# Performance work log

Measured on AMD Instinct MI355X. Metric: run time of the kernel, lower is better.

The kernel has to match this reference:

```python
import jax, jax.numpy as jnp
import numpy as np

DT = 0.1
T_END = 1.0
# matches python `int(t[-1] // dt)` in etd_integration
N_STEPS = int(T_END // DT)


def _expm(X, order=10, squarings=4):
    """Scaling-and-squaring Taylor matrix exponential (fixed order, jit-safe,
    differentiable). Accurate here because ||X|| is kept small by construction."""
    n = X.shape[0]
    I = jnp.eye(n, dtype=X.dtype)
    Xs = X / (2.0 ** squarings)
    term, acc = I, I
    for k in range(1, order + 1):
        term = (term @ Xs) / k
        acc = acc + term
    for _ in range(squarings):
        acc = acc @ acc
    return acc


def etd1_bch2(A, B, dt):
    """ETD1 propagators for dX/dt = A X + X B + N:
    m1_L = e^{dt A}, m1_R = e^{dt B}, m2 = A^{-1}(e^{dt A} - I) (phi1 weight)."""
    m1_L = _expm(dt * A)
    m1_R = _expm(dt * B)
    m2 = jnp.linalg.solve(A, m1_L - jnp.eye(A.shape[0], dtype=A.dtype))
    return m1_L, m1_R, m2


def reference(x, x0, adj, alpha_train, w, d):
    n = adj.shape[0]
    alph = jax.nn.sigmoid(alpha_train)[:, None]          # [n,1]
    d_c = jnp.clip(d, 0.0, 1.0)                          # [2h]
    w_mat = (w * d_c) @ w.T                              # [2h,2h]
    A = alph * 0.5 * adj - alph * 0.5 * jnp.eye(n, dtype=adj.dtype)   # [n,n]
    B = w_mat - jnp.eye(w_mat.shape[0], dtype=w_mat.dtype)            # [2h,2h]
    m1_L, m1_R, m2 = etd1_bch2(A, B, DT)
    forcing = m2 @ x0                                     # constant per step

    def step(IC, _):
        return m1_L @ IC @ m1_R + forcing, None

    z, _ = jax.lax.scan(step, x, None, length=N_STEPS)
    return z


def setup_inputs() -> dict:
    key = jax.random.key(0)
    ks = jax.random.split(key, 6)
    n, dfeat = 2048, 1024
    x = jax.random.normal(ks[0], (n, dfeat), dtype=jnp.float32)
    x0 = jax.random.normal(ks[1], (n, dfeat), dtype=jnp.float32)
    # normalized-adjacency stand-in: uniform entries scaled by 1/n (row sums ~0.5)
    adj = jax.random.uniform(ks[2], (n, n), dtype=jnp.float32) / n
    alpha_train = jax.random.normal(ks[3], (n,), dtype=jnp.float32)
    # original inits w = eye(2h); perturb slightly so math is nontrivial but e^{dtB} stays tame
    w = jnp.eye(dfeat, dtype=jnp.float32) + 0.02 * jax.random.normal(ks[4], (dfeat, dfeat), dtype=jnp.float32)
    d = jax.random.uniform(ks[5], (dfeat,), dtype=jnp.float32)
    return {"x": x, "x0": x0, "adj": adj, "alpha_train": alpha_train, "w": w, "d": d}
```

## Files before the change

kernel.cpp:

```cpp
#include <hip/hip_runtime.h>

typedef __attribute__((ext_vector_type(8))) short short8v;
typedef __attribute__((ext_vector_type(4))) float f32x4;

typedef const __attribute__((address_space(1))) void gvoid_t;
typedef __attribute__((address_space(3))) void svoid_t;

__device__ __forceinline__ unsigned short f2b(float f) {
    unsigned u = __float_as_uint(f);
    unsigned r = (u + 0x7fffu + ((u >> 16) & 1u)) >> 16;
    return (unsigned short)r;
}
__device__ __forceinline__ float b2f(unsigned short h) {
    return __uint_as_float((unsigned)h << 16);
}


__global__ void k_build_A(const float* __restrict__ adj,
                          const float* __restrict__ alpha,
                          float* __restrict__ Xs, unsigned short* __restrict__ Xb,
                          int n, float scale)
{
    int j = blockIdx.x * 256 + threadIdx.x;
    int i = blockIdx.y;
    if (j >= n) return;
    size_t idx = (size_t)i * n + j;
    float s = 1.f / (1.f + expf(-alpha[i]));
    float v = scale * s * (adj[idx] - (i == j ? 1.f : 0.f));
    Xs[idx] = v;
    Xb[idx] = f2b(v);
}

__global__ void k_build_EW(const float* __restrict__ w,
                           const float* __restrict__ d,
                           unsigned short* __restrict__ Eb,
                           unsigned short* __restrict__ Edb,
                           float* __restrict__ Edf, int h)
{
    int j = blockIdx.x * 256 + threadIdx.x;
    int i = blockIdx.y;
    if (j >= h) return;
    size_t idx = (size_t)i * h + j;
    float e = w[idx] - (i == j ? 1.f : 0.f);
    float dc = fminf(fmaxf(d[j], 0.f), 1.f);
    Eb[idx] = f2b(e);
    float ed = e * dc;
    Edb[idx] = f2b(ed);
    Edf[idx] = ed;
}

__global__ void k_build_R(const float* __restrict__ Ed,
                          const float* __restrict__ d,
                          float* __restrict__ R, int h, float dt)
{
    __shared__ float tile[32][33];
    int bx = blockIdx.x * 32, by = blockIdx.y * 32;
    int tx = threadIdx.x, ty = threadIdx.y;
    #pragma unroll
    for (int r = 0; r < 32; r += 8)
        tile[ty + r][tx] = Ed[(size_t)(bx + ty + r) * h + by + tx];
    __syncthreads();
    #pragma unroll
    for (int r = 0; r < 32; r += 8) {
        int i = by + ty + r, j = bx + tx;
        float v = Ed[(size_t)i * h + j] + tile[tx][ty + r];
        if (i == j) v += fminf(fmaxf(d[i], 0.f), 1.f) - 1.f;
        R[(size_t)i * h + j] = dt * v;
    }
}

__global__ void k_tsplit(const float* __restrict__ in,
                         unsigned short* __restrict__ outT, int R, int C)
{
    __shared__ float tile[32][33];
    int bx = blockIdx.x * 32, by = blockIdx.y * 32;
    int tx = threadIdx.x, ty = threadIdx.y;
    #pragma unroll
    for (int r = 0; r < 32; r += 8)
        tile[ty + r][tx] = in[(size_t)(by + ty + r) * C + bx + tx];
    __syncthreads();
    #pragma unroll
    for (int r = 0; r < 32; r += 8)
        outT[(size_t)(bx + ty + r) * R + by + tx] = f2b(tile[tx][ty + r]);
}


template<int FM, int FN, int MW>
__global__ __launch_bounds__(256, MW)
void gemm_bf16(const unsigned short* __restrict__ A,
               const unsigned short* __restrict__ BT,
               float* __restrict__ C,
               float* __restrict__ C2,
               unsigned short* __restrict__ Cb,
               unsigned short* __restrict__ Cb2,
               unsigned short* __restrict__ Cb3,
               unsigned short* __restrict__ CbT,
               const float* __restrict__ D,
               const float* __restrict__ D2,
               const unsigned short* __restrict__ Db,
               int M, int N, int K,
               float alpha, float beta, float g2, float g3,
               float pa, float pb, float pc,
               float qa, float qb, float qc)
{
    constexpr int BM = FM * 32, BN = FN * 32, BK = 64;
    constexpr int AIT = BM * BK / (8 * 256);
    constexpr int BIT = BN * BK / (8 * 256);
    constexpr int LPT = AIT + BIT;
    __shared__ unsigned short As[2][BM * BK];
    __shared__ unsigned short Bs[2][BN * BK];

    int bid = blockIdx.y * gridDim.x + blockIdx.x;
    int rpx = gridDim.y >> 3;
    int q = bid & 7, c = bid >> 3;
    int by = q * rpx + (c % rpx);
    int bx = c / rpx;

    const int tid  = threadIdx.x;
    const int lane = tid & 63;
    const int wave = tid >> 6;
    const int wr = wave >> 1, wc = wave & 1;
    const int l16 = lane & 15, l4 = lane >> 4;
    const int brow = by * BM, bcol = bx * BN;

    f32x4 acc[FM][FN];
    #pragma unroll
    for (int m = 0; m < FM; ++m)
        #pragma unroll
        for (int j = 0; j < FN; ++j)
            acc[m][j] = (f32x4){0.f, 0.f, 0.f, 0.f};

    const unsigned short* Ab = A + (size_t)brow * K;
    const unsigned short* Bb = BT + (size_t)bcol * K;
    const int nt = K / BK;

    auto stage = [&](int b, int k0) {
        #pragma unroll
        for (int it = 0; it < AIT; ++it) {
            int cb = it * 256 + wave * 64;
            int ch = cb + lane;
            int r = ch >> 3, cc = ch & 7;
            int cs = cc ^ (r & 7);
            __builtin_amdgcn_global_load_lds(
                (gvoid_t*)(Ab + (size_t)r * K + k0 + cs * 8),
                (svoid_t*)(&As[b][cb * 8]), 16, 0, 0);
        }
        #pragma unroll
        for (int it = 0; it < BIT; ++it) {
            int cb = it * 256 + wave * 64;
            int ch = cb + lane;
            int r = ch >> 3, cc = ch & 7;
            int cs = cc ^ (r & 7);
            __builtin_amdgcn_global_load_lds(
                (gvoid_t*)(Bb + (size_t)r * K + k0 + cs * 8),
                (svoid_t*)(&Bs[b][cb * 8]), 16, 0, 0);
        }
    };

    stage(0, 0);
    stage(1, BK);

    for (int t = 0; t < nt; ++t) {
        const int cur = t & 1;
        if (t + 1 < nt) {
            asm volatile("s_waitcnt vmcnt(%0)" :: "i"(LPT) : "memory");
        } else {
            asm volatile("s_waitcnt vmcnt(0)" ::: "memory");
        }
        __builtin_amdgcn_s_barrier();
        asm volatile("" ::: "memory");
        __builtin_amdgcn_sched_barrier(0);

        short8v af[FM][2], bf[FN][2];
        #pragma unroll
        for (int m = 0; m < FM; ++m) {
            int r = wr * FM * 16 + m * 16 + l16;
            #pragma unroll
            for (int hf = 0; hf < 2; ++hf) {
                int cs = (hf * 4 + l4) ^ (r & 7);
                af[m][hf] = *(const short8v*)&As[cur][r * BK + cs * 8];
            }
        }
        #pragma unroll
        for (int j = 0; j < FN; ++j) {
            int r = wc * FN * 16 + j * 16 + l16;
            #pragma unroll
            for (int hf = 0; hf < 2; ++hf) {
                int cs = (hf * 4 + l4) ^ (r & 7);
                bf[j][hf] = *(const short8v*)&Bs[cur][r * BK + cs * 8];
            }
        }
        __builtin_amdgcn_s_setprio(1);
        #pragma unroll
        for (int hf = 0; hf < 2; ++hf)
            #pragma unroll
            for (int m = 0; m < FM; ++m)
                #pragma unroll
                for (int j = 0; j < FN; ++j)
                    acc[m][j] = __builtin_amdgcn_mfma_f32_16x16x32_bf16(
                        af[m][hf], bf[j][hf], acc[m][j], 0, 0, 0);
        __builtin_amdgcn_s_setprio(0);
        __builtin_amdgcn_sched_barrier(0);
        __builtin_amdgcn_s_barrier();
        asm volatile("" ::: "memory");
        if (t + 2 < nt) stage(cur, (t + 2) * BK);
    }

    #pragma unroll
    for (int m = 0; m < FM; ++m) {
        #pragma unroll
        for (int j = 0; j < FN; ++j) {
            const int row0 = brow + wr * FM * 16 + m * 16 + l4 * 4;
            const int col  = bcol + wc * FN * 16 + j * 16 + l16;
            float vv[4];
            #pragma unroll
            for (int q2 = 0; q2 < 4; ++q2) {
                size_t idx = (size_t)(row0 + q2) * N + col;
                float a0 = acc[m][j][q2];
                float v = alpha * a0;
                float dv = 0.f, dbv = 0.f;
                if (D)  { dv = D[idx]; v = fmaf(beta, dv, v); }
                if (D2) v = fmaf(g2, D2[idx], v);
                if (Db) { dbv = b2f(Db[idx]); v = fmaf(g3, dbv, v); }
                vv[q2] = v;
                if (C)  C[idx] = v;
                if (Cb) Cb[idx] = f2b(v);
                if (C2 || Cb2) {
                    float v2 = pa * a0;
                    if (D)  v2 = fmaf(pb, dv, v2);
                    if (Db) v2 = fmaf(pc, dbv, v2);
                    if (C2)  C2[idx] = v2;
                    if (Cb2) Cb2[idx] = f2b(v2);
                }
                if (Cb3) {
                    float v3 = qa * a0;
                    if (D)  v3 = fmaf(qb, dv, v3);
                    if (Db) v3 = fmaf(qc, dbv, v3);
                    Cb3[idx] = f2b(v3);
                }
            }
            if (CbT) {
                ushort4 t4;
                t4.x = f2b(vv[0]); t4.y = f2b(vv[1]);
                t4.z = f2b(vv[2]); t4.w = f2b(vv[3]);
                *reinterpret_cast<ushort4*>(&CbT[(size_t)col * M + row0]) = t4;
            }
        }
    }
}


extern "C" void kernel_launch(void* const* d_in, const int* in_sizes, int n_in,
                              void* d_out, int out_size, void* d_ws, size_t ws_size,
                              hipStream_t stream)
{
    const float* x     = (const float*)d_in[0];
    const float* x0    = (const float*)d_in[1];
    const float* adj   = (const float*)d_in[2];
    const float* alpha = (const float*)d_in[3];
    const float* w     = (const float*)d_in[4];
    const float* dvec  = (const float*)d_in[5];

    const int n = in_sizes[3];
    const int h = in_sizes[5];
    const size_t MB = 1u << 20;
    char* ws = (char*)d_ws;

    typedef unsigned short u16;
    float* Xs    = (float*)(ws + 0 * MB);
    u16*   XAb   = (u16*)(ws + 16 * MB);
    u16*   XAT   = (u16*)(ws + 24 * MB);
    u16*   Mah   = (u16*)(ws + 32 * MB);
    u16*   Pmb   = (u16*)(ws + 40 * MB);
    u16*   M3ah  = (u16*)(ws + 48 * MB);
    u16*   MbT   = (u16*)(ws + 56 * MB);
    u16*   M3bTb = (u16*)(ws + 58 * MB);
    u16*   Eb_   = (u16*)(ws + 0 * MB);
    u16*   Edb   = (u16*)(ws + 2 * MB);
    float* Edf   = (float*)(ws + 4 * MB);
    float* R     = (float*)(ws + 8 * MB);
    float* XBf   = (float*)(ws + 12 * MB);
    u16*   XBb   = (u16*)(ws + 16 * MB);
    u16*   XBT   = (u16*)(ws + 18 * MB);
    float* P2f   = (float*)(ws + 20 * MB);
    u16*   P2b   = (u16*)(ws + 24 * MB);
    float* P3f   = (float*)(ws + 26 * MB);
    u16*   P3b   = (u16*)(ws + 30 * MB);
    u16*   x0T   = (u16*)(ws + 0 * MB);
    float* Ff    = (float*)(ws + 4 * MB);
    u16*   FTb   = (u16*)(ws + 12 * MB);
    float* uf    = (float*)(ws + 16 * MB);
    u16*   ub    = (u16*)(ws + 24 * MB);
    float* F2f   = (float*)(ws + 60 * MB);
    u16*   F2Tb  = (u16*)(ws + 12 * MB);
    float* vf    = (float*)(ws + 16 * MB);
    u16*   vb    = (u16*)(ws + 24 * MB);
    float* F3f   = (float*)(ws + 40 * MB);
    u16*   zt    = (u16*)(ws + 68 * MB);
    float* tf    = (float*)(ws + 0 * MB);
    u16*   tb16  = (u16*)(ws + 8 * MB);
    float* za    = (float*)(ws + 16 * MB);

    const dim3 blk(256);
    const dim3 gNN(n / 32, n / 64);
    const dim3 gHN(h / 32, n / 64);
    const dim3 gHH(h / 64, h / 32);
    const float dt = 0.1f;
    const u16* nu16 = nullptr;
    const float* nf32 = nullptr;

    k_build_A<<<dim3(n / 256, n), blk, 0, stream>>>(adj, alpha, Xs, XAb, n, 0.5f * dt);
    k_tsplit<<<dim3(n / 32, n / 32), dim3(32, 8), 0, stream>>>(Xs, XAT, n, n);
    gemm_bf16<2, 1, 4><<<gNN, blk, 0, stream>>>(
        XAb, XAT, nullptr, nullptr, Mah, Pmb, M3ah, nullptr, Xs, nf32, nu16,
        n, n, n, 0.5f, 1.f, 0.f, 0.f,
        1.f / 6.f, 0.5f, 0.f, 4.5f, 3.f, 0.f);

    k_build_EW<<<dim3(h / 256, h), blk, 0, stream>>>(w, dvec, Eb_, Edb, Edf, h);
    k_build_R<<<dim3(h / 32, h / 32), dim3(32, 8), 0, stream>>>(Edf, dvec, R, h, dt);
    gemm_bf16<1, 2, 4><<<gHH, blk, 0, stream>>>(
        Edb, Eb_, XBf, nullptr, XBb, nullptr, nullptr, XBT, R, nf32, nu16,
        h, h, h, dt, 1.f, 0.f, 0.f, 0.f, 0.f, 0.f, 0.f, 0.f, 0.f);
    gemm_bf16<1, 2, 4><<<gHH, blk, 0, stream>>>(
        XBb, XBT, P2f, nullptr, P2b, nullptr, nullptr, nullptr, nf32, nf32, nu16,
        h, h, h, 1.f, 0.f, 0.f, 0.f, 0.f, 0.f, 0.f, 0.f, 0.f, 0.f);
    gemm_bf16<1, 2, 4><<<gHH, blk, 0, stream>>>(
        P2b, XBT, nullptr, P3f, nullptr, P3b, nullptr, MbT, XBf, P2f, nu16,
        h, h, h, 1.f / 6.f, 1.f, 0.5f, 0.f, 1.f, 0.f, 0.f, 0.f, 0.f, 0.f);
    gemm_bf16<1, 2, 4><<<gHH, blk, 0, stream>>>(
        P3b, XBT, nullptr, nullptr, nullptr, nullptr, nullptr, M3bTb,
        P3f, P2f, XBb,
        h, h, h, 3.375f, 4.5f, 4.5f, 3.f, 0.f, 0.f, 0.f, 0.f, 0.f, 0.f);

    k_tsplit<<<dim3(h / 32, n / 32), dim3(32, 8), 0, stream>>>(x0, x0T, n, h);
    gemm_bf16<2, 1, 4><<<gHN, blk, 0, stream>>>(
        Pmb, x0T, Ff, nullptr, nullptr, nullptr, nullptr, FTb, x0, nf32, nu16,
        n, h, n, dt, dt, 0.f, 0.f, 0.f, 0.f, 0.f, 0.f, 0.f, 0.f);
    gemm_bf16<2, 1, 4><<<gHN, blk, 0, stream>>>(
        Mah, FTb, uf, nullptr, ub, nullptr, nullptr, nullptr, Ff, nf32, nu16,
        n, h, n, 1.f, 1.f, 0.f, 0.f, 0.f, 0.f, 0.f, 0.f, 0.f, 0.f);
    gemm_bf16<2, 1, 4><<<gHN, blk, 0, stream>>>(
        ub, MbT, F2f, nullptr, nullptr, nullptr, nullptr, F2Tb, uf, Ff, nu16,
        n, h, h, 1.f, 1.f, 1.f, 0.f, 0.f, 0.f, 0.f, 0.f, 0.f, 0.f);
    gemm_bf16<2, 1, 4><<<gHN, blk, 0, stream>>>(
        Mah, F2Tb, vf, nullptr, vb, nullptr, nullptr, nullptr, F2f, nf32, nu16,
        n, h, n, 1.f, 1.f, 0.f, 0.f, 0.f, 0.f, 0.f, 0.f, 0.f, 0.f);
    gemm_bf16<2, 1, 4><<<gHN, blk, 0, stream>>>(
        vb, MbT, F3f, nullptr, nullptr, nullptr, nullptr, nullptr, vf, Ff, nu16,
        n, h, h, 1.f, 1.f, 1.f, 0.f, 0.f, 0.f, 0.f, 0.f, 0.f, 0.f);

    k_tsplit<<<dim3(h / 32, n / 32), dim3(32, 8), 0, stream>>>(x, zt, n, h);
    const float* zf = x;
    for (int s = 0; s < 3; ++s) {
        gemm_bf16<2, 1, 4><<<gHN, blk, 0, stream>>>(
            M3ah, zt, tf, nullptr, tb16, nullptr, nullptr, nullptr, zf, nf32, nu16,
            n, h, n, 1.f, 1.f, 0.f, 0.f, 0.f, 0.f, 0.f, 0.f, 0.f, 0.f);
        float* zout = (s == 2) ? (float*)d_out : za;
        gemm_bf16<2, 1, 4><<<gHN, blk, 0, stream>>>(
            tb16, M3bTb, zout, nullptr, nullptr, nullptr, nullptr,
            (s == 2) ? nullptr : zt, tf, F3f, nu16,
            n, h, h, 1.f, 1.f, 1.f, 0.f, 0.f, 0.f, 0.f, 0.f, 0.f, 0.f);
        zf = za;
    }
}
```

Measured before the change: 353.0 us.

## Fuse A build with transpose, merge x/x0 transposes, read bf16 epilogue operands

Builds the scaled A matrix and its bf16 transpose in a single tiled kernel instead of writing an fp32 copy and transposing it separately. The x0 and x transposes are merged into one launch. Several GEMM epilogues now take the bf16 residual copy instead of fp32 intermediates, so fp32 outputs such as uf, vf and tf are no longer written or read. The n×n GEMM moves to a 2×2 fragment tile, and workspace offsets are repacked. This cuts memory traffic and launch count, but residual terms are now added at bf16 rather than fp32 precision, which costs accuracy.

```diff
diff --git a/kernel.cpp b/kernel.cpp
--- a/kernel.cpp
+++ b/kernel.cpp
@@ -16,19 +16,27 @@
 }
 
 
-__global__ void k_build_A(const float* __restrict__ adj,
-                          const float* __restrict__ alpha,
-                          float* __restrict__ Xs, unsigned short* __restrict__ Xb,
-                          int n, float scale)
-{
-    int j = blockIdx.x * 256 + threadIdx.x;
-    int i = blockIdx.y;
-    if (j >= n) return;
-    size_t idx = (size_t)i * n + j;
-    float s = 1.f / (1.f + expf(-alpha[i]));
-    float v = scale * s * (adj[idx] - (i == j ? 1.f : 0.f));
-    Xs[idx] = v;
-    Xb[idx] = f2b(v);
+__global__ void k_build_AT(const float* __restrict__ adj,
+                           const float* __restrict__ alpha,
+                           unsigned short* __restrict__ XAb,
+                           unsigned short* __restrict__ XATb,
+                           int n, float scale)
+{
+    __shared__ float tile[32][33];
+    int bx = blockIdx.x * 32, by = blockIdx.y * 32;
+    int tx = threadIdx.x, ty = threadIdx.y;
+    #pragma unroll
+    for (int r = 0; r < 32; r += 8) {
+        int i = by + ty + r, j = bx + tx;
+        float s = 1.f / (1.f + expf(-alpha[i]));
+        float v = scale * s * (adj[(size_t)i * n + j] - (i == j ? 1.f : 0.f));
+        XAb[(size_t)i * n + j] = f2b(v);
+        tile[ty + r][tx] = v;
+    }
+    __syncthreads();
+    #pragma unroll
+    for (int r = 0; r < 32; r += 8)
+        XATb[(size_t)(bx + ty + r) * n + by + tx] = f2b(tile[tx][ty + r]);
 }
 
 __global__ void k_build_EW(const float* __restrict__ w,
@@ -69,19 +77,29 @@
     }
 }
 
-__global__ void k_tsplit(const float* __restrict__ in,
-                         unsigned short* __restrict__ outT, int R, int C)
+__global__ void k_tsplit2(const float* __restrict__ in0,
+                          const float* __restrict__ in1,
+                          unsigned short* __restrict__ out0,
+                          unsigned short* __restrict__ out1, int R, int C)
 {
     __shared__ float tile[32][33];
     int bx = blockIdx.x * 32, by = blockIdx.y * 32;
     int tx = threadIdx.x, ty = threadIdx.y;
     #pragma unroll
     for (int r = 0; r < 32; r += 8)
-        tile[ty + r][tx] = in[(size_t)(by + ty + r) * C + bx + tx];
-    __syncthreads();
-    #pragma unroll
-    for (int r = 0; r < 32; r += 8)
-        outT[(size_t)(bx + ty + r) * R + by + tx] = f2b(tile[tx][ty + r]);
+        tile[ty + r][tx] = in0[(size_t)(by + ty + r) * C + bx + tx];
+    __syncthreads();
+    #pragma unroll
+    for (int r = 0; r < 32; r += 8)
+        out0[(size_t)(bx + ty + r) * R + by + tx] = f2b(tile[tx][ty + r]);
+    __syncthreads();
+    #pragma unroll
+    for (int r = 0; r < 32; r += 8)
+        tile[ty + r][tx] = in1[(size_t)(by + ty + r) * C + bx + tx];
+    __syncthreads();
+    #pragma unroll
+    for (int r = 0; r < 32; r += 8)
+        out1[(size_t)(bx + ty + r) * R + by + tx] = f2b(tile[tx][ty + r]);
 }
 
 
@@ -267,54 +285,51 @@
     char* ws = (char*)d_ws;
 
     typedef unsigned short u16;
-    float* Xs    = (float*)(ws + 0 * MB);
-    u16*   XAb   = (u16*)(ws + 16 * MB);
-    u16*   XAT   = (u16*)(ws + 24 * MB);
-    u16*   Mah   = (u16*)(ws + 32 * MB);
-    u16*   Pmb   = (u16*)(ws + 40 * MB);
-    u16*   M3ah  = (u16*)(ws + 48 * MB);
-    u16*   MbT   = (u16*)(ws + 56 * MB);
-    u16*   M3bTb = (u16*)(ws + 58 * MB);
+    u16*   XAb   = (u16*)(ws + 0 * MB);
+    u16*   XATb  = (u16*)(ws + 8 * MB);
+    u16*   Mah   = (u16*)(ws + 16 * MB);
+    u16*   Pmb   = (u16*)(ws + 24 * MB);
+    u16*   M3ah  = (u16*)(ws + 32 * MB);
+    u16*   MbT   = (u16*)(ws + 40 * MB);
+    u16*   M3bTb = (u16*)(ws + 42 * MB);
     u16*   Eb_   = (u16*)(ws + 0 * MB);
     u16*   Edb   = (u16*)(ws + 2 * MB);
     float* Edf   = (float*)(ws + 4 * MB);
     float* R     = (float*)(ws + 8 * MB);
     float* XBf   = (float*)(ws + 12 * MB);
-    u16*   XBb   = (u16*)(ws + 16 * MB);
-    u16*   XBT   = (u16*)(ws + 18 * MB);
-    float* P2f   = (float*)(ws + 20 * MB);
-    u16*   P2b   = (u16*)(ws + 24 * MB);
-    float* P3f   = (float*)(ws + 26 * MB);
-    u16*   P3b   = (u16*)(ws + 30 * MB);
+    u16*   XBb   = (u16*)(ws + 44 * MB);
+    u16*   XBT   = (u16*)(ws + 46 * MB);
+    float* P2f   = (float*)(ws + 48 * MB);
+    u16*   P2b   = (u16*)(ws + 52 * MB);
+    float* P3f   = (float*)(ws + 54 * MB);
+    u16*   P3b   = (u16*)(ws + 58 * MB);
     u16*   x0T   = (u16*)(ws + 0 * MB);
     float* Ff    = (float*)(ws + 4 * MB);
-    u16*   FTb   = (u16*)(ws + 12 * MB);
-    float* uf    = (float*)(ws + 16 * MB);
-    u16*   ub    = (u16*)(ws + 24 * MB);
-    float* F2f   = (float*)(ws + 60 * MB);
-    u16*   F2Tb  = (u16*)(ws + 12 * MB);
-    float* vf    = (float*)(ws + 16 * MB);
-    u16*   vb    = (u16*)(ws + 24 * MB);
-    float* F3f   = (float*)(ws + 40 * MB);
-    u16*   zt    = (u16*)(ws + 68 * MB);
-    float* tf    = (float*)(ws + 0 * MB);
-    u16*   tb16  = (u16*)(ws + 8 * MB);
-    float* za    = (float*)(ws + 16 * MB);
+    u16*   Fb    = (u16*)(ws + 12 * MB);
+    u16*   FTb   = (u16*)(ws + 44 * MB);
+    u16*   ub    = (u16*)(ws + 48 * MB);
+    u16*   F2b   = (u16*)(ws + 52 * MB);
+    u16*   F2Tb  = (u16*)(ws + 56 * MB);
+    u16*   vb    = (u16*)(ws + 60 * MB);
+    float* F3f   = (float*)(ws + 64 * MB);
+    u16*   zt    = (u16*)(ws + 72 * MB);
+    u16*   tb16  = (u16*)(ws + 76 * MB);
+    float* za    = (float*)(ws + 80 * MB);
 
     const dim3 blk(256);
-    const dim3 gNN(n / 32, n / 64);
+    const dim3 gNN(n / 64, n / 64);
     const dim3 gHN(h / 32, n / 64);
     const dim3 gHH(h / 64, h / 32);
     const float dt = 0.1f;
     const u16* nu16 = nullptr;
     const float* nf32 = nullptr;
 
-    k_build_A<<<dim3(n / 256, n), blk, 0, stream>>>(adj, alpha, Xs, XAb, n, 0.5f * dt);
-    k_tsplit<<<dim3(n / 32, n / 32), dim3(32, 8), 0, stream>>>(Xs, XAT, n, n);
-    gemm_bf16<2, 1, 4><<<gNN, blk, 0, stream>>>(
-        XAb, XAT, nullptr, nullptr, Mah, Pmb, M3ah, nullptr, Xs, nf32, nu16,
-        n, n, n, 0.5f, 1.f, 0.f, 0.f,
-        1.f / 6.f, 0.5f, 0.f, 4.5f, 3.f, 0.f);
+    k_build_AT<<<dim3(n / 32, n / 32), dim3(32, 8), 0, stream>>>(
+        adj, alpha, XAb, XATb, n, 0.5f * dt);
+    gemm_bf16<2, 2, 4><<<gNN, blk, 0, stream>>>(
+        XAb, XATb, nullptr, nullptr, Mah, Pmb, M3ah, nullptr, nf32, nf32, XAb,
+        n, n, n, 0.5f, 0.f, 0.f, 1.f,
+        1.f / 6.f, 0.f, 0.5f, 4.5f, 0.f, 3.f);
 
     k_build_EW<<<dim3(h / 256, h), blk, 0, stream>>>(w, dvec, Eb_, Edb, Edf, h);
     k_build_R<<<dim3(h / 32, h / 32), dim3(32, 8), 0, stream>>>(Edf, dvec, R, h, dt);
@@ -332,34 +347,36 @@
         P3f, P2f, XBb,
         h, h, h, 3.375f, 4.5f, 4.5f, 3.f, 0.f, 0.f, 0.f, 0.f, 0.f, 0.f);
 
-    k_tsplit<<<dim3(h / 32, n / 32), dim3(32, 8), 0, stream>>>(x0, x0T, n, h);
-    gemm_bf16<2, 1, 4><<<gHN, blk, 0, stream>>>(
-        Pmb, x0T, Ff, nullptr, nullptr, nullptr, nullptr, FTb, x0, nf32, nu16,
+    k_tsplit2<<<dim3(h / 32, n / 32), dim3(32, 8), 0, stream>>>(
+        x0, x, x0T, zt, n, h);
+
+    gemm_bf16<2, 1, 4><<<gHN, blk, 0, stream>>>(
+        Pmb, x0T, Ff, nullptr, Fb, nullptr, nullptr, FTb, x0, nf32, nu16,
         n, h, n, dt, dt, 0.f, 0.f, 0.f, 0.f, 0.f, 0.f, 0.f, 0.f);
     gemm_bf16<2, 1, 4><<<gHN, blk, 0, stream>>>(
-        Mah, FTb, uf, nullptr, ub, nullptr, nullptr, nullptr, Ff, nf32, nu16,
-        n, h, n, 1.f, 1.f, 0.f, 0.f, 0.f, 0.f, 0.f, 0.f, 0.f, 0.f);
-    gemm_bf16<2, 1, 4><<<gHN, blk, 0, stream>>>(
-        ub, MbT, F2f, nullptr, nullptr, nullptr, nullptr, F2Tb, uf, Ff, nu16,
-        n, h, h, 1.f, 1.f, 1.f, 0.f, 0.f, 0.f, 0.f, 0.f, 0.f, 0.f);
-    gemm_bf16<2, 1, 4><<<gHN, blk, 0, stream>>>(
-        Mah, F2Tb, vf, nullptr, vb, nullptr, nullptr, nullptr, F2f, nf32, nu16,
-        n, h, n, 1.f, 1.f, 0.f, 0.f, 0.f, 0.f, 0.f, 0.f, 0.f, 0.f);
-    gemm_bf16<2, 1, 4><<<gHN, blk, 0, stream>>>(
-        vb, MbT, F3f, nullptr, nullptr, nullptr, nullptr, nullptr, vf, Ff, nu16,
-        n, h, h, 1.f, 1.f, 1.f, 0.f, 0.f, 0.f, 0.f, 0.f, 0.f, 0.f);
-
-    k_tsplit<<<dim3(h / 32, n / 32), dim3(32, 8), 0, stream>>>(x, zt, n, h);
+        Mah, FTb, nullptr, nullptr, ub, nullptr, nullptr, nullptr, nf32, nf32, Fb,
+        n, h, n, 1.f, 0.f, 0.f, 1.f, 0.f, 0.f, 0.f, 0.f, 0.f, 0.f);
+    gemm_bf16<2, 1, 4><<<gHN, blk, 0, stream>>>(
+        ub, MbT, nullptr, nullptr, F2b, nullptr, nullptr, F2Tb, nf32, Ff, ub,
+        n, h, h, 1.f, 0.f, 1.f, 1.f, 0.f, 0.f, 0.f, 0.f, 0.f, 0.f);
+    gemm_bf16<2, 1, 4><<<gHN, blk, 0, stream>>>(
+        Mah, F2Tb, nullptr, nullptr, vb, nullptr, nullptr, nullptr, nf32, nf32, F2b,
+        n, h, n, 1.f, 0.f, 0.f, 1.f, 0.f, 0.f, 0.f, 0.f, 0.f, 0.f);
+    gemm_bf16<2, 1, 4><<<gHN, blk, 0, stream>>>(
+        vb, MbT, F3f, nullptr, nullptr, nullptr, nullptr, nullptr, nf32, Ff, vb,
+        n, h, h, 1.f, 0.f, 1.f, 1.f, 0.f, 0.f, 0.f, 0.f, 0.f, 0.f);
+
     const float* zf = x;
     for (int s = 0; s < 3; ++s) {
         gemm_bf16<2, 1, 4><<<gHN, blk, 0, stream>>>(
-            M3ah, zt, tf, nullptr, tb16, nullptr, nullptr, nullptr, zf, nf32, nu16,
+            M3ah, zt, nullptr, nullptr, tb16, nullptr, nullptr, nullptr,
+            zf, nf32, nu16,
             n, h, n, 1.f, 1.f, 0.f, 0.f, 0.f, 0.f, 0.f, 0.f, 0.f, 0.f);
         float* zout = (s == 2) ? (float*)d_out : za;
         gemm_bf16<2, 1, 4><<<gHN, blk, 0, stream>>>(
             tb16, M3bTb, zout, nullptr, nullptr, nullptr, nullptr,
-            (s == 2) ? nullptr : zt, tf, F3f, nu16,
-            n, h, h, 1.f, 1.f, 1.f, 0.f, 0.f, 0.f, 0.f, 0.f, 0.f, 0.f);
+            (s == 2) ? nullptr : zt, nf32, F3f, tb16,
+            n, h, h, 1.f, 0.f, 1.f, 1.f, 0.f, 0.f, 0.f, 0.f, 0.f, 0.f);
         zf = za;
     }
 }
```

After: 323.2 us. 8.5% less time.
